# Kernel tuning notes

Hardware: AMD Instinct MI355X
Metric: run time of the kernel (lower is better)

## Reference

```python
import jax, jax.numpy as jnp
import numpy as np

R = 32          # voxel resolution
GROUPS = 8
EPS = 1e-5


def silu(x):
    return x * jax.nn.sigmoid(x)


def group_norm(x, gamma, beta):
    # x: (B, C, *spatial); normalize over (C/G, *spatial) per group
    B, C = x.shape[0], x.shape[1]
    sp = x.shape[2:]
    xg = x.reshape(B, GROUPS, C // GROUPS, -1)
    mean = xg.mean(axis=(2, 3), keepdims=True)
    var = xg.var(axis=(2, 3), keepdims=True)
    xn = ((xg - mean) * jax.lax.rsqrt(var + EPS)).reshape(B, C, *sp)
    pshape = (1, C) + (1,) * len(sp)
    return xn * gamma.reshape(pshape) + beta.reshape(pshape)


def voxelize(x, coords):
    # x: (B, C, N), coords: (B, N, 3) in [0, 1] -> scatter-mean onto (B, C, R, R, R)
    c = coords * (R - 1)
    idx = jnp.clip(jnp.floor(c).astype(jnp.int32), 0, R - 1)
    flat = (idx[..., 0] * R + idx[..., 1]) * R + idx[..., 2]  # (B, N)

    def one(feat_cn, fi):
        sums = jax.ops.segment_sum(feat_cn.T, fi, num_segments=R ** 3)        # (R^3, C)
        cnt = jax.ops.segment_sum(jnp.ones_like(fi, dtype=feat_cn.dtype), fi,
                                  num_segments=R ** 3)                        # (R^3,)
        mean = sums / jnp.clip(cnt, 1.0)[:, None]
        return mean.T.reshape(feat_cn.shape[0], R, R, R)

    return jax.vmap(one)(x, flat)


def devoxelize(vox, coords):
    # vox: (B, C, R, R, R), coords: (B, N, 3) -> trilinear gather (B, C, N)
    B, C = vox.shape[0], vox.shape[1]
    c = coords * (R - 1)
    f = c - jnp.floor(c)                                  # fractional part (B, N, 3)
    x0 = jnp.clip(jnp.floor(c).astype(jnp.int32), 0, R - 1)
    x1 = jnp.clip(x0 + 1, 0, R - 1)
    vflat = vox.reshape(B, C, R ** 3)
    out = jnp.zeros((B, C, coords.shape[1]), dtype=vox.dtype)
    for dx in (0, 1):
        for dy in (0, 1):
            for dz in (0, 1):
                ix = x1[..., 0] if dx else x0[..., 0]
                iy = x1[..., 1] if dy else x0[..., 1]
                iz = x1[..., 2] if dz else x0[..., 2]
                w = ((f[..., 0] if dx else 1.0 - f[..., 0])
                     * (f[..., 1] if dy else 1.0 - f[..., 1])
                     * (f[..., 2] if dz else 1.0 - f[..., 2]))  # (B, N)
                fi = (ix * R + iy) * R + iz                      # (B, N)
                g = jnp.take_along_axis(vflat, fi[:, None, :], axis=2)  # (B, C, N)
                out = out + g * w[:, None, :]
    return out


def conv3d(x, w):
    # x: (B, C, D, H, W), w: (O, I, 3, 3, 3), padding 1
    return jax.lax.conv_general_dilated(
        x, w, window_strides=(1, 1, 1), padding='SAME',
        dimension_numbers=('NCDHW', 'OIDHW', 'NCDHW'))


def setup_inputs() -> dict:
    key = jax.random.key(0)
    ks = jax.random.split(key, 16)
    B, Cin, Cout, N, T = 4, 32, 64, 32768, 256
    s = 0.02
    return {
        'feats_bcn': jax.random.normal(ks[0], (B, Cin, N), jnp.float32),
        'coords_bnc3': jax.random.uniform(ks[1], (B, N, 3), jnp.float32),
        't_emb_bt': jax.random.normal(ks[2], (B, T), jnp.float32),
        'w_in': jax.random.normal(ks[3], (Cout, Cin), jnp.float32) * s,
        'gn1_g': jnp.ones((Cout,), jnp.float32), 'gn1_b': jnp.zeros((Cout,), jnp.float32),
        'w_time': jax.random.normal(ks[4], (Cout, T), jnp.float32) * s,
        'b_time': jnp.zeros((Cout,), jnp.float32),
        'w_vox1': jax.random.normal(ks[5], (Cout, Cout, 3, 3, 3), jnp.float32) * s,
        'gn2_g': jnp.ones((Cout,), jnp.float32), 'gn2_b': jnp.zeros((Cout,), jnp.float32),
        'w_vox2': jax.random.normal(ks[6], (Cout, Cout, 3, 3, 3), jnp.float32) * s,
        'gn3_g': jnp.ones((Cout,), jnp.float32), 'gn3_b': jnp.zeros((Cout,), jnp.float32),
        'w_fuse': jax.random.normal(ks[7], (Cout, Cout), jnp.float32) * s,
        'gn4_g': jnp.ones((Cout,), jnp.float32), 'gn4_b': jnp.zeros((Cout,), jnp.float32),
        'w_skip': jax.random.normal(ks[8], (Cout, Cin), jnp.float32) * s,
    }


def reference(feats_bcn, coords_bnc3, t_emb_bt, w_in, gn1_g, gn1_b, w_time, b_time,
              w_vox1, gn2_g, gn2_b, w_vox2, gn3_g, gn3_b, w_fuse, gn4_g, gn4_b, w_skip):
    # point_in: 1x1 conv1d + GN + SiLU
    x_in = silu(group_norm(jnp.einsum('oc,bcn->bon', w_in, feats_bcn), gn1_g, gn1_b))
    # time bias
    bias = (t_emb_bt @ w_time.T + b_time)[:, :, None]          # (B, C, 1)
    x_in = x_in + bias
    # scatter-mean voxelization + bias
    vox = voxelize(x_in, coords_bnc3) + bias[..., None, None]  # (B, C, R, R, R)
    # voxel conv stack
    vox = silu(group_norm(conv3d(vox, w_vox1), gn2_g, gn2_b))
    vox = silu(group_norm(conv3d(vox, w_vox2), gn3_g, gn3_b))
    # trilinear devoxelize back to points
    devox = devoxelize(vox, coords_bnc3)                        # (B, C, N)
    out = silu(group_norm(jnp.einsum('oc,bcn->bon', w_fuse, devox), gn4_g, gn4_b))
    x_skip = jnp.einsum('oc,bcn->bon', w_skip, feats_bcn)
    return out + x_skip
```

## Files before the change

### kernel.cpp

```cpp
#include <hip/hip_runtime.h>
#include <hip/hip_bf16.h>
#include <hip/hip_fp16.h>

typedef __hip_bfloat16 bf16;
typedef unsigned short u16;
typedef unsigned int u32;
typedef __attribute__((ext_vector_type(8))) short bf16x8;
typedef __attribute__((ext_vector_type(4))) float f32x4;

#define DI __device__ __forceinline__

DI float bfu2f(u32 u) { u32 v = u << 16; float f; __builtin_memcpy(&f, &v, 4); return f; }
DI u16 f2bfu(float f) { bf16 h = __float2bfloat16(f); u16 u; __builtin_memcpy(&u, &h, 2); return u; }
DI float hu2f(u32 u) { __half h; u16 s = (u16)u; __builtin_memcpy(&h, &s, 2); return __half2float(h); }
DI u16 f2hu(float f) { __half h = __float2half(f); u16 u; __builtin_memcpy(&u, &h, 2); return u; }
DI float silu_f(float x) { return x / (1.0f + __expf(-x)); }
DI float ldin(const void* p, long i, int bf) {
  return bf ? bfu2f(((const u16*)p)[i]) : ((const float*)p)[i];
}
DI int detect_bf(const void* g) { return ((*(const u32*)g) & 0xFFFFu) == 0x3F80u; }
DI void unpack8(uint4 q, float* o) {
  o[0] = bfu2f(q.x & 0xFFFFu); o[1] = bfu2f(q.x >> 16);
  o[2] = bfu2f(q.y & 0xFFFFu); o[3] = bfu2f(q.y >> 16);
  o[4] = bfu2f(q.z & 0xFFFFu); o[5] = bfu2f(q.z >> 16);
  o[6] = bfu2f(q.w & 0xFFFFu); o[7] = bfu2f(q.w >> 16);
}
DI void unpack8h(uint4 q, float* o) {
  o[0] = hu2f(q.x & 0xFFFFu); o[1] = hu2f(q.x >> 16);
  o[2] = hu2f(q.y & 0xFFFFu); o[3] = hu2f(q.y >> 16);
  o[4] = hu2f(q.z & 0xFFFFu); o[5] = hu2f(q.z >> 16);
  o[6] = hu2f(q.w & 0xFFFFu); o[7] = hu2f(q.w >> 16);
}
DI uint4 pack8(const float* s) {
  uint4 q;
  q.x = (u32)f2bfu(s[0]) | ((u32)f2bfu(s[1]) << 16);
  q.y = (u32)f2bfu(s[2]) | ((u32)f2bfu(s[3]) << 16);
  q.z = (u32)f2bfu(s[4]) | ((u32)f2bfu(s[5]) << 16);
  q.w = (u32)f2bfu(s[6]) | ((u32)f2bfu(s[7]) << 16);
  return q;
}


__global__ void k_prep(const void* __restrict__ w_in, const void* __restrict__ w_fuse,
                       const void* __restrict__ w_skip, const void* __restrict__ wv1,
                       const void* __restrict__ wv2,
                       const void* __restrict__ g1g, const void* __restrict__ g1b,
                       const void* __restrict__ g2g, const void* __restrict__ g2b,
                       const void* __restrict__ g3g, const void* __restrict__ g3b,
                       const void* __restrict__ g4g, const void* __restrict__ g4b,
                       const void* __restrict__ t_emb, const void* __restrict__ w_time,
                       const void* __restrict__ b_time,
                       float* __restrict__ wT_in, float* __restrict__ wT_fuse,
                       float* __restrict__ wT_skip, u16* __restrict__ wM1,
                       u16* __restrict__ wM2, float* __restrict__ gnp,
                       u16* __restrict__ wFuseM, float* __restrict__ biasb) {
  int bf = detect_bf(g1g);
  int id = blockIdx.x * 256 + threadIdx.x;
  if (id < 2048) { int c = id >> 6, o = id & 63; wT_in[id] = ldin(w_in, o * 32 + c, bf); return; }
  id -= 2048;
  if (id < 4096) { int o = id >> 6, p = id & 63; wT_fuse[id] = ldin(w_fuse, p * 64 + o, bf); return; }
  id -= 4096;
  if (id < 2048) { int c = id >> 6, p = id & 63; wT_skip[id] = ldin(w_skip, p * 32 + c, bf); return; }
  id -= 2048;
  if (id < 110592) {
    int c = id & 63, o = (id >> 6) & 63, t = id >> 12;
    int g = t / 3, t2 = t - g * 3;
    wM1[g * 12288 + ((((t2 * 64 + o) << 6) + c) ^ ((o & 7) << 3))] =
        f2bfu(ldin(wv1, (o * 64 + c) * 27 + t, bf));
    return;
  }
  id -= 110592;
  if (id < 110592) {
    int c = id & 63, o = (id >> 6) & 63, t = id >> 12;
    int g = t / 3, t2 = t - g * 3;
    wM2[g * 12288 + ((((t2 * 64 + o) << 6) + c) ^ ((o & 7) << 3))] =
        f2bfu(ldin(wv2, (o * 64 + c) * 27 + t, bf));
    return;
  }
  id -= 110592;
  if (id < 512) {
    int stage = id >> 7, j = id & 127;
    const void* src;
    if (stage == 0) src = (j < 64) ? g1g : g1b;
    else if (stage == 1) src = (j < 64) ? g2g : g2b;
    else if (stage == 2) src = (j < 64) ? g3g : g3b;
    else src = (j < 64) ? g4g : g4b;
    gnp[id] = ldin(src, j & 63, bf);
    return;
  }
  id -= 512;
  if (id < 4096) {
    int kh = id >> 11, nt = (id >> 9) & 3, l = (id >> 3) & 63, j = id & 7;
    int o = nt * 16 + (l & 15);
    int k = kh * 32 + ((l >> 4) & 3) * 8 + j;
    wFuseM[id] = f2bfu(ldin(w_fuse, o * 64 + k, bf));
    return;
  }
  id -= 4096;
  if (id < 256) {
    int b = id >> 6, o = id & 63;
    float s = ldin(b_time, o, bf);
    for (int t = 0; t < 256; ++t)
      s += ldin(t_emb, b * 256 + t, bf) * ldin(w_time, o * 256 + t, bf);
    biasb[id] = s;
  }
}

__global__ void k_points(const void* __restrict__ coords, int4* __restrict__ pt4,
                         int* __restrict__ pt_vox, int* __restrict__ counts,
                         const void* __restrict__ g1g) {
  int bf = detect_bf(g1g);
  int id = blockIdx.x * 256 + threadIdx.x;
  int b = id >> 15;
  float cx = ldin(coords, (long)id * 3 + 0, bf) * 31.f;
  float cy = ldin(coords, (long)id * 3 + 1, bf) * 31.f;
  float cz = ldin(coords, (long)id * 3 + 2, bf) * 31.f;
  int x0 = min(max((int)floorf(cx), 0), 31);
  int y0 = min(max((int)floorf(cy), 0), 31);
  int z0 = min(max((int)floorf(cz), 0), 31);
  int x1 = min(x0 + 1, 31), y1 = min(y0 + 1, 31), z1 = min(z0 + 1, 31);
  int pack = x0 | (y0 << 5) | (z0 << 10) | (x1 << 15) | (y1 << 20) | (z1 << 25);
  int4 r;
  r.x = pack;
  float fx = cx - floorf(cx), fy = cy - floorf(cy), fz = cz - floorf(cz);
  __builtin_memcpy(&r.y, &fx, 4);
  __builtin_memcpy(&r.z, &fy, 4);
  __builtin_memcpy(&r.w, &fz, 4);
  pt4[id] = r;
  int fi = (x0 << 10) + (y0 << 5) + z0;
  int bv = (b << 15) + fi;
  pt_vox[id] = bv;
  atomicAdd(counts + bv, 1);
}

__global__ void k_scan1(const int* __restrict__ cnt, int* __restrict__ starts,
                        int* __restrict__ bsum) {
  __shared__ int ls[256];
  int t = threadIdx.x;
  int base = blockIdx.x * 1024 + t * 4;
  int4 c = *(const int4*)(cnt + base);
  int s = c.x + c.y + c.z + c.w;
  ls[t] = s;
  __syncthreads();
  for (int off = 1; off < 256; off <<= 1) {
    int u = (t >= off) ? ls[t - off] : 0;
    __syncthreads();
    ls[t] += u;
    __syncthreads();
  }
  int excl = ls[t] - s;
  starts[base] = excl;
  starts[base + 1] = excl + c.x;
  starts[base + 2] = excl + c.x + c.y;
  starts[base + 3] = excl + c.x + c.y + c.z;
  if (t == 255) bsum[blockIdx.x] = ls[255];
}

__global__ void k_scan3(int* __restrict__ starts, const int* __restrict__ bsum,
                        int* __restrict__ cursor) {
  __shared__ int bp[128];
  int t = threadIdx.x;
  int v0 = (t < 128) ? bsum[t] : 0;
  if (t < 128) bp[t] = v0;
  __syncthreads();
  for (int off = 1; off < 128; off <<= 1) {
    int u = (t >= off && t < 128) ? bp[t - off] : 0;
    __syncthreads();
    if (t < 128) bp[t] += u;
    __syncthreads();
  }
  if (t < 128) bp[t] -= v0;
  __syncthreads();
  int i = blockIdx.x * 256 + t;
  int v = starts[i] + bp[i >> 10];
  starts[i] = v;
  cursor[i] = v;
}

__global__ void k_fill(const int* __restrict__ pt_vox, const int4* __restrict__ pt4,
                       int* __restrict__ cursor, int* __restrict__ list,
                       int4* __restrict__ ptS, int* __restrict__ pid2slot) {
  int id = blockIdx.x * 256 + threadIdx.x;
  int slot = atomicAdd(cursor + pt_vox[id], 1);
  list[slot] = id;
  ptS[slot] = pt4[id];
  pid2slot[id] = slot;
}

__global__ void __launch_bounds__(256, 2) k_xin(const void* __restrict__ feats,
                      const float* __restrict__ wT_in, const int* __restrict__ pid2slot,
                      u16* __restrict__ out, float* __restrict__ gs,
                      const void* __restrict__ g1g) {
  __shared__ float xs[4][16];
  int bf = detect_bf(g1g);
  int tid = threadIdx.x;
  int id = blockIdx.x * 256 + tid;
  int b = id >> 15, n = id & 32767;
  float acc[64];
#pragma unroll
  for (int o = 0; o < 64; ++o) acc[o] = 0.f;
  long base = ((long)b << 20) + n;
  for (int c = 0; c < 32; ++c) {
    float fv = ldin(feats, base + ((long)c << 15), bf);
    const float* wr = wT_in + (c << 6);
#pragma unroll
    for (int o = 0; o < 64; ++o) acc[o] += wr[o] * fv;
  }
  int slot = pid2slot[id];
  uint4* op = (uint4*)(out + ((size_t)slot << 6));
#pragma unroll
  for (int j = 0; j < 8; ++j) op[j] = pack8(acc + j * 8);
  float ps[8], pq[8];
#pragma unroll
  for (int g = 0; g < 8; ++g) {
    float s = 0.f, q = 0.f;
#pragma unroll
    for (int k = 0; k < 8; ++k) { float v = acc[g * 8 + k]; s += v; q += v * v; }
    ps[g] = s; pq[g] = q;
  }
#pragma unroll
  for (int m = 1; m < 64; m <<= 1)
#pragma unroll
    for (int g = 0; g < 8; ++g) {
      ps[g] += __shfl_xor(ps[g], m);
      pq[g] += __shfl_xor(pq[g], m);
    }
  int lane = tid & 63, wv = tid >> 6;
  if (lane == 0) {
#pragma unroll
    for (int g = 0; g < 8; ++g) { xs[wv][g * 2] = ps[g]; xs[wv][g * 2 + 1] = pq[g]; }
  }
  __syncthreads();
  if (tid < 16) {
    float t = xs[0][tid] + xs[1][tid] + xs[2][tid] + xs[3][tid];
    atomicAdd(gs + (blockIdx.x & 7) * 64 + ((b * 8 + (tid >> 1)) << 1) + (tid & 1), t);
  }
}

DI void stats_inline(const float* __restrict__ gsumB, int b, int tid, float* st) {
  if (tid < 8) {
    float s = 0.f, q = 0.f;
    int bg = b * 8 + tid;
#pragma unroll
    for (int bin = 0; bin < 8; ++bin) {
      s += gsumB[bin * 64 + bg * 2];
      q += gsumB[bin * 64 + bg * 2 + 1];
    }
    float mean = s * (1.0f / 262144.0f);
    float var = q * (1.0f / 262144.0f) - mean * mean;
    st[tid * 2] = mean;
    st[tid * 2 + 1] = rsqrtf(fmaxf(var, 0.f) + 1e-5f);
  }
}

__global__ void k_gather(const u16* __restrict__ xmulS, const int* __restrict__ starts,
                         const int* __restrict__ cnt, const float* __restrict__ gsumB,
                         const float* __restrict__ gnp0,
                         const float* __restrict__ bias, u16* __restrict__ voxout) {
  __shared__ float st[16];
  int tid = threadIdx.x;
  int id = blockIdx.x * 256 + tid;
  int j = id & 7;
  int bv = id >> 3;
  int b = bv >> 15;
  stats_inline(gsumB, b, tid, st);
  __syncthreads();
  int s = starts[bv], c = cnt[bv];
  float m = st[j * 2], r = st[j * 2 + 1];
  float acc[8] = {0.f, 0.f, 0.f, 0.f, 0.f, 0.f, 0.f, 0.f};
  for (int k = 0; k < c; ++k) {
    uint4 q = *(const uint4*)(xmulS + ((size_t)(s + k) << 6) + j * 8);
    float x[8];
    unpack8(q, x);
#pragma unroll
    for (int t = 0; t < 8; ++t)
      acc[t] += silu_f((x[t] - m) * r * gnp0[j * 8 + t] + gnp0[64 + j * 8 + t]);
  }
  float inv = 1.0f / fmaxf((float)c, 1.0f);
  float bmul = c ? 2.0f : 1.0f;
  float out[8];
#pragma unroll
  for (int t = 0; t < 8; ++t)
    out[t] = acc[t] * inv + bmul * bias[b * 64 + j * 8 + t];
  *(uint4*)(voxout + ((size_t)bv << 6) + j * 8) = pack8(out);
}

__global__ void __launch_bounds__(256, 3) k_mconv(const u16* __restrict__ in,
                                                  const u16* __restrict__ wM,
                                                  u16* __restrict__ out,
                                                  const u16* __restrict__ zrow,
                                                  float* __restrict__ gs) {
  __shared__ u16 wlds[2][12288];
  int orig = blockIdx.x;
  int wid = (orig & 7) * 128 + (orig >> 3);
  int bin = orig & 7;
  int b = wid >> 8;
  int a0 = (wid >> 3) & 31;
  int a1row0 = (wid & 7) << 2;
  int tid = threadIdx.x;
  int wave = tid >> 6, lane = tid & 63;
  int quad = lane >> 4, lrow = lane & 15;
  int a1row = a1row0 + wave;
  const u16* inb = in + ((size_t)b << 21);
  const u16* zp = zrow + quad * 8;
  f32x4 acc[2][4] = {};

  auto stage = [&](int it, int bufi) {
    const u16* src = wM + it * 12288;
    u16* dst = &wlds[bufi][0];
    for (int ch = wave; ch < 24; ch += 4)
      __builtin_amdgcn_global_load_lds(
          (const __attribute__((address_space(1))) void*)(src + ch * 512 + lane * 8),
          (__attribute__((address_space(3))) void*)(dst + ch * 512), 16, 0, 0);
  };

  stage(0, 0);
#pragma unroll 1
  for (int it = 0; it < 9; ++it) {
    int t0 = it / 3;
    int t1 = it - t0 * 3;
    int n0 = a0 + t0 - 1;
    bool rowok = (unsigned)n0 < 32u;
    int n0c = min(max(n0, 0), 31);
    int n1 = a1row + t1 - 1;
    bool n1ok = (unsigned)n1 < 32u;
    int n1c = min(max(n1, 0), 31);
    bf16x8 areg[3][2][2];
#pragma unroll
    for (int t2 = 0; t2 < 3; ++t2) {
#pragma unroll
      for (int mt = 0; mt < 2; ++mt) {
        int n2 = mt * 16 + lrow + t2 - 1;
        bool sel = rowok && n1ok && ((unsigned)n2 < 32u);
        int n2c = min(max(n2, 0), 31);
        const u16* rp = inb + ((size_t)((n0c << 10) + (n1c << 5) + n2c) << 6) + quad * 8;
        const u16* ap = sel ? rp : zp;
        areg[t2][mt][0] = *(const bf16x8*)(ap);
        areg[t2][mt][1] = *(const bf16x8*)(ap + 32);
      }
    }
    __builtin_amdgcn_sched_barrier(0);
    if (it < 8) {
      stage(it + 1, (it + 1) & 1);
      asm volatile("s_waitcnt vmcnt(18)" ::: "memory");
    } else {
      asm volatile("s_waitcnt vmcnt(12)" ::: "memory");
    }
    __builtin_amdgcn_s_barrier();
    const u16* wb = &wlds[it & 1][0];
    int swz = (lrow & 7) << 3;
    __builtin_amdgcn_s_setprio(1);
#pragma unroll
    for (int t2 = 0; t2 < 3; ++t2) {
      bf16x8 wf[2][4];
#pragma unroll
      for (int kh = 0; kh < 2; ++kh)
#pragma unroll
        for (int nt = 0; nt < 4; ++nt)
          wf[kh][nt] = *(const bf16x8*)(wb +
              ((((t2 * 64 + nt * 16 + lrow) << 6) + kh * 32 + quad * 8) ^ swz));
#pragma unroll
      for (int mt = 0; mt < 2; ++mt)
#pragma unroll
        for (int kh = 0; kh < 2; ++kh)
#pragma unroll
          for (int nt = 0; nt < 4; ++nt)
            acc[mt][nt] = __builtin_amdgcn_mfma_f32_16x16x32_bf16(
                areg[t2][mt][kh], wf[kh][nt], acc[mt][nt], 0, 0, 0);
    }
    __builtin_amdgcn_s_setprio(0);
    __builtin_amdgcn_s_barrier();
  }

  size_t vbase = ((size_t)b << 15) + (a0 << 10) + (a1row << 5);
#pragma unroll
  for (int mt = 0; mt < 2; ++mt) {
#pragma unroll
    for (int nt = 0; nt < 4; ++nt)
#pragma unroll
      for (int r = 0; r < 4; ++r)
        out[((vbase + mt * 16 + quad * 4 + r) << 6) + nt * 16 + lrow] = f2hu(acc[mt][nt][r]);
  }

  float s[4], q[4];
#pragma unroll
  for (int nt = 0; nt < 4; ++nt) {
    float ss = 0.f, qq = 0.f;
#pragma unroll
    for (int mt = 0; mt < 2; ++mt)
#pragma unroll
      for (int r = 0; r < 4; ++r) { float v = acc[mt][nt][r]; ss += v; qq += v * v; }
    s[nt] = ss; q[nt] = qq;
  }
#pragma unroll
  for (int mi = 0; mi < 5; ++mi) {
    const int masks[5] = {1, 2, 4, 16, 32};
    int m = masks[mi];
#pragma unroll
    for (int nt = 0; nt < 4; ++nt) {
      s[nt] += __shfl_xor(s[nt], m);
      q[nt] += __shfl_xor(q[nt], m);
    }
  }
  __syncthreads();
  float* fs = (float*)&wlds[0][0];
  int par = lrow >> 3;
  if (quad == 0 && (lrow & 7) == 0) {
#pragma unroll
    for (int nt = 0; nt < 4; ++nt) {
      fs[wave * 16 + ((nt * 2 + par) << 1)] = s[nt];
      fs[wave * 16 + ((nt * 2 + par) << 1) + 1] = q[nt];
    }
  }
  __syncthreads();
  if (tid < 16) {
    float t = fs[tid] + fs[16 + tid] + fs[32 + tid] + fs[48 + tid];
    atomicAdd(gs + bin * 64 + ((b * 8 + (tid >> 1)) << 1) + (tid & 1), t);
  }
}

__global__ void k_gnapply(const u16* __restrict__ src, const float* __restrict__ gsumB,
                          const float* __restrict__ gnp, u16* __restrict__ dst) {
  __shared__ float st[16];
  int tid = threadIdx.x;
  int id = blockIdx.x * 256 + tid;
  int j = id & 7;
  int bv = id >> 3;
  int b = bv >> 15;
  stats_inline(gsumB, b, tid, st);
  __syncthreads();
  const u16* ip = src + ((size_t)bv << 6) + j * 8;
  float x[8];
  unpack8h(*(const uint4*)ip, x);
  float m = st[j * 2], r = st[j * 2 + 1];
#pragma unroll
  for (int k = 0; k < 8; ++k)
    x[k] = silu_f((x[k] - m) * r * gnp[j * 8 + k] + gnp[64 + j * 8 + k]);
  *(uint4*)(dst + ((size_t)bv << 6) + j * 8) = pack8(x);
}

__global__ void __launch_bounds__(256, 4) k_devoxfuse(const u16* __restrict__ vox,
                       const int4* __restrict__ ptS, const int* __restrict__ list,
                       const u16* __restrict__ wFuseM,
                       u16* __restrict__ dst, float* __restrict__ gs) {
  __shared__ int lsl[256];
  __shared__ float fsh[4][16];
  int tid = threadIdx.x;
  int wave = tid >> 6, lane = tid & 63;
  int quad = lane >> 4, lrow = lane & 15;
  int blk = blockIdx.x;
  int b = blk >> 7;
  int bin = blk & 7;
  lsl[tid] = list[blk * 256 + tid];
  bf16x8 bF[2][4];
#pragma unroll
  for (int kh = 0; kh < 2; ++kh)
#pragma unroll
    for (int nt = 0; nt < 4; ++nt)
      bF[kh][nt] = *(const bf16x8*)(wFuseM + ((kh * 4 + nt) * 64 + lane) * 8);
  __syncthreads();
  const u16* vb = vox + ((size_t)b << 21) + quad * 8;
  float sr[4] = {0.f, 0.f, 0.f, 0.f}, qr[4] = {0.f, 0.f, 0.f, 0.f};

#pragma unroll 1
  for (int i = 0; i < 4; ++i) {
    int sbase = blk * 256 + wave * 64 + i * 16;
    int4 pt = ptS[sbase + lrow];
    int pk = pt.x;
    int x0 = pk & 31, y0 = (pk >> 5) & 31, z0 = (pk >> 10) & 31;
    int x1 = (pk >> 15) & 31, y1 = (pk >> 20) & 31, z1 = (pk >> 25) & 31;
    float fx, fy, fz;
    __builtin_memcpy(&fx, &pt.y, 4);
    __builtin_memcpy(&fy, &pt.z, 4);
    __builtin_memcpy(&fz, &pt.w, 4);
    float facc[16];
#pragma unroll
    for (int t = 0; t < 16; ++t) facc[t] = 0.f;
#pragma unroll
    for (int dx = 0; dx < 2; ++dx) {
      int ixc = dx ? x1 : x0;
      float wx = dx ? fx : 1.f - fx;
#pragma unroll
      for (int dy = 0; dy < 2; ++dy) {
        int iyc = dy ? y1 : y0;
        float wxy = wx * (dy ? fy : 1.f - fy);
#pragma unroll
        for (int dz = 0; dz < 2; ++dz) {
          int izc = dz ? z1 : z0;
          float w = wxy * (dz ? fz : 1.f - fz);
          const u16* p = vb + ((size_t)((ixc << 10) + (iyc << 5) + izc) << 6);
          float v0[8], v1[8];
          unpack8(*(const uint4*)p, v0);
          unpack8(*(const uint4*)(p + 32), v1);
#pragma unroll
          for (int t = 0; t < 8; ++t) { facc[t] += w * v0[t]; facc[8 + t] += w * v1[t]; }
        }
      }
    }
    bf16x8 a0, a1;
#pragma unroll
    for (int t = 0; t < 8; ++t) {
      a0[t] = (short)f2bfu(facc[t]);
      a1[t] = (short)f2bfu(facc[8 + t]);
    }
    f32x4 acc4[4] = {};
#pragma unroll
    for (int nt = 0; nt < 4; ++nt)
      acc4[nt] = __builtin_amdgcn_mfma_f32_16x16x32_bf16(a0, bF[0][nt], acc4[nt], 0, 0, 0);
#pragma unroll
    for (int nt = 0; nt < 4; ++nt)
      acc4[nt] = __builtin_amdgcn_mfma_f32_16x16x32_bf16(a1, bF[1][nt], acc4[nt], 0, 0, 0);
    int4 pids = *(const int4*)&lsl[wave * 64 + i * 16 + quad * 4];
    int pid_[4] = {pids.x, pids.y, pids.z, pids.w};
#pragma unroll
    for (int nt = 0; nt < 4; ++nt) {
#pragma unroll
      for (int r = 0; r < 4; ++r) {
        float v = acc4[nt][r];
        dst[((size_t)pid_[r] << 6) + nt * 16 + lrow] = f2bfu(v);
        sr[nt] += v; qr[nt] += v * v;
      }
    }
  }

#pragma unroll
  for (int mi = 0; mi < 5; ++mi) {
    const int masks[5] = {1, 2, 4, 16, 32};
    int m = masks[mi];
#pragma unroll
    for (int nt = 0; nt < 4; ++nt) {
      sr[nt] += __shfl_xor(sr[nt], m);
      qr[nt] += __shfl_xor(qr[nt], m);
    }
  }
  int par = lrow >> 3;
  if (quad == 0 && (lrow & 7) == 0) {
#pragma unroll
    for (int nt = 0; nt < 4; ++nt) {
      fsh[wave][(nt * 2 + par) << 1] = sr[nt];
      fsh[wave][((nt * 2 + par) << 1) + 1] = qr[nt];
    }
  }
  __syncthreads();
  if (tid < 16) {
    float t = fsh[0][tid] + fsh[1][tid] + fsh[2][tid] + fsh[3][tid];
    atomicAdd(gs + bin * 64 + ((b * 8 + (tid >> 1)) << 1) + (tid & 1), t);
  }
}

__global__ void __launch_bounds__(256, 2) k_final(const u16* __restrict__ y,
                        const float* __restrict__ gsumB,
                        const float* __restrict__ gnp3, const void* __restrict__ feats,
                        const float* __restrict__ wT_skip, float* __restrict__ out,
                        const void* __restrict__ g1g) {
  __shared__ float st[16];
  int bf = detect_bf(g1g);
  int tid = threadIdx.x;
  int id = blockIdx.x * 256 + tid;
  int b = id >> 15, n = id & 32767;
  stats_inline(gsumB, b, tid, st);
  __syncthreads();
  const uint4* yr = (const uint4*)(y + ((size_t)id << 6));
  float r[64];
#pragma unroll
  for (int j = 0; j < 8; ++j) unpack8(yr[j], r + j * 8);
#pragma unroll
  for (int o = 0; o < 64; ++o) {
    int g = o >> 3;
    r[o] = silu_f((r[o] - st[g * 2]) * st[g * 2 + 1] * gnp3[o] + gnp3[64 + o]);
  }
  long base = ((long)b << 20) + n;
  for (int c = 0; c < 32; ++c) {
    float fv = ldin(feats, base + ((long)c << 15), bf);
    const float* wr = wT_skip + (c << 6);
#pragma unroll
    for (int p = 0; p < 64; ++p) r[p] += wr[p] * fv;
  }
  float* op = out + ((size_t)b << 21) + n;
#pragma unroll
  for (int p = 0; p < 64; ++p) op[(size_t)p << 15] = r[p];
}

extern "C" void kernel_launch(void* const* d_in, const int* in_sizes, int n_in,
                              void* d_out, int out_size, void* d_ws, size_t ws_size,
                              hipStream_t stream) {
  const void* feats  = d_in[0];
  const void* coords = d_in[1];
  const void* t_emb  = d_in[2];
  const void* w_in   = d_in[3];
  const void* gn1_g  = d_in[4];
  const void* gn1_b  = d_in[5];
  const void* w_time = d_in[6];
  const void* b_time = d_in[7];
  const void* w_vox1 = d_in[8];
  const void* gn2_g  = d_in[9];
  const void* gn2_b  = d_in[10];
  const void* w_vox2 = d_in[11];
  const void* gn3_g  = d_in[12];
  const void* gn3_b  = d_in[13];
  const void* w_fuse = d_in[14];
  const void* gn4_g  = d_in[15];
  const void* gn4_b  = d_in[16];
  const void* w_skip = d_in[17];

  u16* S = (u16*)d_out;

  char* ws = (char*)d_ws;
  u16*   BufP    = (u16*)  (ws + 0);
  u16*   VoxB    = (u16*)  (ws + 16777216);
  int*   counts  = (int*)  (ws + 33554432);
  float* gsumB   = (float*)(ws + 34078720);
  u16*   zpad    = (u16*)  (ws + 34086912);
  int4*  pt4     = (int4*) (ws + 34087168);
  int*   pt_vox  = (int*)  (ws + 36184320);
  int*   starts  = (int*)  (ws + 36708608);
  int*   cursor  = (int*)  (ws + 37232896);
  int*   list    = (int*)  (ws + 37757184);
  int4*  ptS     = (int4*) (ws + 38281472);
  int*   bsum    = (int*)  (ws + 40378624);
  float* biasb   = (float*)(ws + 40379136);
  float* gnp     = (float*)(ws + 40380160);
  float* wT_in   = (float*)(ws + 40382208);
  float* wT_fuse = (float*)(ws + 40390400);
  float* wT_skip = (float*)(ws + 40406784);
  u16*   wM1     = (u16*)  (ws + 40414976);
  u16*   wM2     = (u16*)  (ws + 40636160);
  u16*   wFuseM  = (u16*)  (ws + 40857344);
  int*   pid2slot= (int*)  (ws + 40865536);

  hipMemsetAsync(counts, 0, 532736, stream);

  k_prep<<<915, 256, 0, stream>>>(w_in, w_fuse, w_skip, w_vox1, w_vox2,
                                  gn1_g, gn1_b, gn2_g, gn2_b, gn3_g, gn3_b,
                                  gn4_g, gn4_b, t_emb, w_time, b_time,
                                  wT_in, wT_fuse, wT_skip, wM1, wM2, gnp,
                                  wFuseM, biasb);
  k_points<<<512, 256, 0, stream>>>(coords, pt4, pt_vox, counts, gn1_g);
  k_scan1<<<128, 256, 0, stream>>>(counts, starts, bsum);
  k_scan3<<<512, 256, 0, stream>>>(starts, bsum, cursor);
  k_fill<<<512, 256, 0, stream>>>(pt_vox, pt4, cursor, list, ptS, pid2slot);
  k_xin<<<512, 256, 0, stream>>>(feats, wT_in, pid2slot, BufP, gsumB + 0, gn1_g);
  k_gather<<<4096, 256, 0, stream>>>(BufP, starts, counts, gsumB + 0,
                                     gnp + 0, biasb, VoxB);
  k_mconv<<<1024, 256, 0, stream>>>(VoxB, wM1, S, zpad, gsumB + 512);
  k_gnapply<<<4096, 256, 0, stream>>>(S, gsumB + 512, gnp + 128, BufP);
  k_mconv<<<1024, 256, 0, stream>>>(BufP, wM2, S, zpad, gsumB + 1024);
  k_gnapply<<<4096, 256, 0, stream>>>(S, gsumB + 1024, gnp + 256, VoxB);
  k_devoxfuse<<<512, 256, 0, stream>>>(VoxB, ptS, list, wFuseM, BufP, gsumB + 1536);
  k_final<<<512, 256, 0, stream>>>(BufP, gsumB + 1536, gnp + 384, feats, wT_skip,
                                   (float*)d_out, gn1_g);
}
```

Baseline: 396.8 us.

## Stage input halo tile in LDS and stream weights from global into registers

The 3D conv kernel now loads the whole input halo (3x6x34 voxel rows) for a block into LDS once, with an XOR swizzle and zero-padding via a zero row. Previously activations were reloaded from global per tap and weights were double-buffered in LDS. Weights are now pre-laid out in MFMA fragment order, so each lane reads them straight from global into registers, prefetched one tap ahead. This removes the redundant global activation loads and the per-iteration barriers. In exchange LDS use grows to about 78 KB, and occupancy drops to 2 blocks per CU.

```diff
diff --git a/kernel.cpp b/kernel.cpp
--- a/kernel.cpp
+++ b/kernel.cpp
@@ -63,18 +63,18 @@
   if (id < 2048) { int c = id >> 6, p = id & 63; wT_skip[id] = ldin(w_skip, p * 32 + c, bf); return; }
   id -= 2048;
   if (id < 110592) {
-    int c = id & 63, o = (id >> 6) & 63, t = id >> 12;
-    int g = t / 3, t2 = t - g * 3;
-    wM1[g * 12288 + ((((t2 * 64 + o) << 6) + c) ^ ((o & 7) << 3))] =
-        f2bfu(ldin(wv1, (o * 64 + c) * 27 + t, bf));
+    int j = id & 7, l = (id >> 3) & 63, f = (id >> 9) & 7, t = id >> 12;
+    int o = (f & 3) * 16 + (l & 15);
+    int c = (f >> 2) * 32 + ((l >> 4) & 3) * 8 + j;
+    wM1[id] = f2bfu(ldin(wv1, (o * 64 + c) * 27 + t, bf));
     return;
   }
   id -= 110592;
   if (id < 110592) {
-    int c = id & 63, o = (id >> 6) & 63, t = id >> 12;
-    int g = t / 3, t2 = t - g * 3;
-    wM2[g * 12288 + ((((t2 * 64 + o) << 6) + c) ^ ((o & 7) << 3))] =
-        f2bfu(ldin(wv2, (o * 64 + c) * 27 + t, bf));
+    int j = id & 7, l = (id >> 3) & 63, f = (id >> 9) & 7, t = id >> 12;
+    int o = (f & 3) * 16 + (l & 15);
+    int c = (f >> 2) * 32 + ((l >> 4) & 3) * 8 + j;
+    wM2[id] = f2bfu(ldin(wv2, (o * 64 + c) * 27 + t, bf));
     return;
   }
   id -= 110592;
@@ -285,92 +285,82 @@
   *(uint4*)(voxout + ((size_t)bv << 6) + j * 8) = pack8(out);
 }
 
-__global__ void __launch_bounds__(256, 3) k_mconv(const u16* __restrict__ in,
+__global__ void __launch_bounds__(256, 2) k_mconv(const u16* __restrict__ in,
                                                   const u16* __restrict__ wM,
                                                   u16* __restrict__ out,
                                                   const u16* __restrict__ zrow,
                                                   float* __restrict__ gs) {
-  __shared__ u16 wlds[2][12288];
+  __shared__ u16 alds[39168];
   int orig = blockIdx.x;
   int wid = (orig & 7) * 128 + (orig >> 3);
   int bin = orig & 7;
   int b = wid >> 8;
   int a0 = (wid >> 3) & 31;
-  int a1row0 = (wid & 7) << 2;
+  int a1base = (wid & 7) << 2;
   int tid = threadIdx.x;
   int wave = tid >> 6, lane = tid & 63;
   int quad = lane >> 4, lrow = lane & 15;
-  int a1row = a1row0 + wave;
+  int a1row = a1base + wave;
   const u16* inb = in + ((size_t)b << 21);
-  const u16* zp = zrow + quad * 8;
   f32x4 acc[2][4] = {};
 
-  auto stage = [&](int it, int bufi) {
-    const u16* src = wM + it * 12288;
-    u16* dst = &wlds[bufi][0];
-    for (int ch = wave; ch < 24; ch += 4)
+  for (int it = 0; it < 20; ++it) {
+    int cbase = it * 256 + wave * 64;
+    int chunk = cbase + lane;
+    if (chunk < 4896) {
+      int r = chunk >> 3, p = chunk & 7;
+      int p0 = r / 204, rem = r - p0 * 204;
+      int p1 = rem / 34, n2i = rem - p1 * 34;
+      int n0 = a0 + p0 - 1, n1 = a1base + p1 - 1, n2 = n2i - 1;
+      bool ok = ((unsigned)n0 < 32u) && ((unsigned)n1 < 32u) && ((unsigned)n2 < 32u);
+      int co = (p ^ (r & 7)) << 3;
+      const u16* src = ok ? inb + (((size_t)((n0 << 10) + (n1 << 5) + n2)) << 6) + co
+                          : zrow + co;
       __builtin_amdgcn_global_load_lds(
-          (const __attribute__((address_space(1))) void*)(src + ch * 512 + lane * 8),
-          (__attribute__((address_space(3))) void*)(dst + ch * 512), 16, 0, 0);
-  };
-
-  stage(0, 0);
+          (const __attribute__((address_space(1))) void*)src,
+          (__attribute__((address_space(3))) void*)(alds + ((size_t)cbase << 3)), 16, 0, 0);
+    }
+  }
+  asm volatile("s_waitcnt vmcnt(0)" ::: "memory");
+  __builtin_amdgcn_s_barrier();
+
+#define LOADW(W, T) { \
+  const u16* wp = wM + ((size_t)(T) << 12) + (lane << 3); \
+  _Pragma("unroll") for (int f = 0; f < 8; ++f) \
+    W[f >> 2][f & 3] = *(const bf16x8*)(wp + (f << 9)); \
+}
+#define COMPUTE(T2, W) { \
+  int rb = (t0 * 6 + wave + t1) * 34 + (T2); \
+  _Pragma("unroll") for (int mt = 0; mt < 2; ++mt) { \
+    int r = rb + mt * 16 + lrow; \
+    int sw = (r & 7) << 3; \
+    const u16* rp = alds + r * 64; \
+    _Pragma("unroll") for (int kh = 0; kh < 2; ++kh) { \
+      bf16x8 a = *(const bf16x8*)(rp + (((kh * 4 + quad) << 3) ^ sw)); \
+      _Pragma("unroll") for (int nt = 0; nt < 4; ++nt) \
+        acc[mt][nt] = __builtin_amdgcn_mfma_f32_16x16x32_bf16(a, W[kh][nt], acc[mt][nt], 0, 0, 0); \
+    } \
+  } \
+}
+
+  bf16x8 w0[2][4], w1[2][4], w2[2][4];
+  LOADW(w0, 0);
+  LOADW(w1, 1);
+  int t0 = 0, t1 = 0;
 #pragma unroll 1
-  for (int it = 0; it < 9; ++it) {
-    int t0 = it / 3;
-    int t1 = it - t0 * 3;
-    int n0 = a0 + t0 - 1;
-    bool rowok = (unsigned)n0 < 32u;
-    int n0c = min(max(n0, 0), 31);
-    int n1 = a1row + t1 - 1;
-    bool n1ok = (unsigned)n1 < 32u;
-    int n1c = min(max(n1, 0), 31);
-    bf16x8 areg[3][2][2];
-#pragma unroll
-    for (int t2 = 0; t2 < 3; ++t2) {
-#pragma unroll
-      for (int mt = 0; mt < 2; ++mt) {
-        int n2 = mt * 16 + lrow + t2 - 1;
-        bool sel = rowok && n1ok && ((unsigned)n2 < 32u);
-        int n2c = min(max(n2, 0), 31);
-        const u16* rp = inb + ((size_t)((n0c << 10) + (n1c << 5) + n2c) << 6) + quad * 8;
-        const u16* ap = sel ? rp : zp;
-        areg[t2][mt][0] = *(const bf16x8*)(ap);
-        areg[t2][mt][1] = *(const bf16x8*)(ap + 32);
-      }
-    }
-    __builtin_amdgcn_sched_barrier(0);
-    if (it < 8) {
-      stage(it + 1, (it + 1) & 1);
-      asm volatile("s_waitcnt vmcnt(18)" ::: "memory");
-    } else {
-      asm volatile("s_waitcnt vmcnt(12)" ::: "memory");
-    }
-    __builtin_amdgcn_s_barrier();
-    const u16* wb = &wlds[it & 1][0];
-    int swz = (lrow & 7) << 3;
-    __builtin_amdgcn_s_setprio(1);
-#pragma unroll
-    for (int t2 = 0; t2 < 3; ++t2) {
-      bf16x8 wf[2][4];
-#pragma unroll
-      for (int kh = 0; kh < 2; ++kh)
-#pragma unroll
-        for (int nt = 0; nt < 4; ++nt)
-          wf[kh][nt] = *(const bf16x8*)(wb +
-              ((((t2 * 64 + nt * 16 + lrow) << 6) + kh * 32 + quad * 8) ^ swz));
-#pragma unroll
-      for (int mt = 0; mt < 2; ++mt)
-#pragma unroll
-        for (int kh = 0; kh < 2; ++kh)
-#pragma unroll
-          for (int nt = 0; nt < 4; ++nt)
-            acc[mt][nt] = __builtin_amdgcn_mfma_f32_16x16x32_bf16(
-                areg[t2][mt][kh], wf[kh][nt], acc[mt][nt], 0, 0, 0);
-    }
-    __builtin_amdgcn_s_setprio(0);
-    __builtin_amdgcn_s_barrier();
-  }
+  for (int g = 0; g < 9; ++g) {
+    int tb = g * 3;
+    LOADW(w2, tb + 2);
+    COMPUTE(0, w0);
+    if (tb + 3 < 27) LOADW(w0, tb + 3);
+    COMPUTE(1, w1);
+    if (tb + 4 < 27) LOADW(w1, tb + 4);
+    COMPUTE(2, w2);
+    ++t1;
+    if (t1 == 3) { t1 = 0; ++t0; }
+  }
+#undef LOADW
+#undef COMPUTE
 
   size_t vbase = ((size_t)b << 15) + (a0 << 10) + (a1row << 5);
 #pragma unroll
@@ -403,7 +393,7 @@
     }
   }
   __syncthreads();
-  float* fs = (float*)&wlds[0][0];
+  float* fs = (float*)&alds[0];
   int par = lrow >> 3;
   if (quad == 0 && (lrow & 7) == 0) {
 #pragma unroll
```

Measured after the change: 342.0 us. 13.8% less time.
